# Kernel tuning notes

Measured on AMD Instinct MI355X. Metric: run time of the kernel, lower is better.

## Reference

```python
import jax, jax.numpy as jnp
import numpy as np

B, N = 128, 1369
DINO, CLIP, H = 384, 512, 8
D = CLIP // H  # head_dim = 64
EPS = 1e-5


def setup_inputs() -> dict:
    key = jax.random.key(0)
    ks = jax.random.split(key, 8)
    s_clip = 1.0 / np.sqrt(CLIP)
    s_dino = 1.0 / np.sqrt(DINO)
    return {
        "dino_features": jax.random.normal(ks[0], (B, N, DINO), jnp.float32),
        "clip_features": jax.random.normal(ks[1], (B, CLIP), jnp.float32),
        "Wq": jax.random.uniform(ks[2], (CLIP, CLIP), jnp.float32, -s_clip, s_clip),
        "bq": jnp.zeros((CLIP,), jnp.float32),
        "Wk": jax.random.uniform(ks[3], (DINO, CLIP), jnp.float32, -s_dino, s_dino),
        "bk": jnp.zeros((CLIP,), jnp.float32),
        "Wv": jax.random.uniform(ks[4], (DINO, CLIP), jnp.float32, -s_dino, s_dino),
        "bv": jnp.zeros((CLIP,), jnp.float32),
        "temperature": jnp.ones((1,), jnp.float32),
        "ln_gamma": jnp.ones((CLIP,), jnp.float32),
        "ln_beta": jnp.zeros((CLIP,), jnp.float32),
    }


def reference(dino_features, clip_features, Wq, bq, Wk, bk, Wv, bv,
              temperature, ln_gamma, ln_beta):
    # Q: (B, H, D) -- single query token from CLIP
    Q = (clip_features @ Wq + bq).reshape(B, H, D)
    # K, V: (B, N, H, D)
    K = (dino_features @ Wk + bk).reshape(B, N, H, D)
    V = (dino_features @ Wv + bv).reshape(B, N, H, D)
    scale = jnp.sqrt(jnp.float32(D)) * temperature[0]
    # attention logits over patches: (B, H, N)
    logits = jnp.einsum("bhd,bnhd->bhn", Q, K) / scale
    attn = jax.nn.softmax(logits, axis=-1)  # dropout is identity in eval mode
    out = jnp.einsum("bhn,bnhd->bhd", attn, V).reshape(B, CLIP)
    # LayerNorm over last dim
    mu = out.mean(axis=-1, keepdims=True)
    var = out.var(axis=-1, keepdims=True)
    return (out - mu) * jax.lax.rsqrt(var + EPS) * ln_gamma + ln_beta
```

## Files before the change

kernel.cpp:

```cpp
#include <hip/hip_runtime.h>
#include <math.h>
#include <stdint.h>

#define B_    128
#define N_    1369
#define DINO_ 384
#define CLIP_ 512
#define H_    8
#define CHUNKS 6
#define CH     229
#define SMP    52
#define TROWS  16

__device__ __forceinline__ float wave_sum(float v) {
  v += __shfl_xor(v, 1);  v += __shfl_xor(v, 2);  v += __shfl_xor(v, 4);
  v += __shfl_xor(v, 8);  v += __shfl_xor(v, 16); v += __shfl_xor(v, 32);
  return v;
}

__device__ __forceinline__ void gld16(const float* g, float* lds_base) {
  __builtin_amdgcn_global_load_lds(
      (const __attribute__((address_space(1))) void*)g,
      (__attribute__((address_space(3))) void*)lds_base, 16, 0, 0);
}

__global__ __launch_bounds__(256) void kq(const float* __restrict__ clip,
                                          const float* __restrict__ Wq,
                                          const float* __restrict__ bq,
                                          float* __restrict__ Q) {
  const int b = blockIdx.x;
  const int c = blockIdx.y * 256 + threadIdx.x;
  __shared__ float cl[CLIP_];
  cl[threadIdx.x] = clip[b * CLIP_ + threadIdx.x];
  cl[threadIdx.x + 256] = clip[b * CLIP_ + threadIdx.x + 256];
  __syncthreads();
  float acc = bq[c];
  #pragma unroll 8
  for (int j = 0; j < CLIP_; ++j) acc += cl[j] * Wq[j * CLIP_ + c];
  Q[b * CLIP_ + c] = acc;
}

__global__ __launch_bounds__(256) void kqk(const float* __restrict__ Wk,
                                           const float* __restrict__ Q,
                                           const float* __restrict__ temp,
                                           float* __restrict__ qkout) {
  const int b = blockIdx.x;
  const int e = blockIdx.y * 256 + threadIdx.x;
  __shared__ float qs[CLIP_];
  qs[threadIdx.x] = Q[b * CLIP_ + threadIdx.x];
  qs[threadIdx.x + 256] = Q[b * CLIP_ + threadIdx.x + 256];
  __syncthreads();
  const int h = e / DINO_;
  const int j = e - h * DINO_;
  const float rs = 1.0f / (8.0f * temp[0]);
  const float* wrow = Wk + (size_t)j * CLIP_ + h * 64;
  const float* qrow = qs + h * 64;
  float a0 = 0.f, a1 = 0.f, a2 = 0.f, a3 = 0.f;
  #pragma unroll
  for (int d = 0; d < 64; d += 4) {
    const float4 wv = *(const float4*)(wrow + d);
    const float4 qv = *(const float4*)(qrow + d);
    a0 += wv.x * qv.x;  a1 += wv.y * qv.y;
    a2 += wv.z * qv.z;  a3 += wv.w * qv.w;
  }
  qkout[(size_t)b * 3072 + e] = ((a0 + a1) + (a2 + a3)) * rs;
}

__global__ __launch_bounds__(256, 3) void kmain(const float* __restrict__ dino,
                                                const float* __restrict__ qk,
                                                float* __restrict__ ps,
                                                float* __restrict__ pl) {
  __shared__ float lds[2 * TROWS * DINO_];
  __shared__ float lm[2][H_];

  const int blk = blockIdx.x;
  const int b = blk / CHUNKS;
  const int c = blk - b * CHUNKS;
  const int n0 = c * CH;
  const int n1 = min(N_, n0 + CH);
  const int tid = threadIdx.x, w = tid >> 6, lane = tid & 63;
  const int h = lane >> 3, sl = lane & 7;
  const int off = 4 * sl;

  float qr[48];
  {
    const float* qb = qk + (size_t)b * 3072 + h * DINO_ + off;
    #pragma unroll
    for (int t = 0; t < 12; ++t) {
      const float4 v = *(const float4*)(qb + 32 * t);
      qr[4*t] = v.x; qr[4*t+1] = v.y; qr[4*t+2] = v.z; qr[4*t+3] = v.w;
    }
  }
  float s[48];
  #pragma unroll
  for (int k = 0; k < 48; ++k) s[k] = 0.0f;
  float l = 0.0f;

  const float* gdino = dino + (size_t)b * N_ * DINO_;
  const float* gclamp = dino + ((size_t)B_ * N_ * DINO_ - 4);
  const int ntiles = (n1 - n0 + TROWS - 1) / TROWS;

  {
    const float* gb = gdino + (size_t)n0 * DINO_;
    #pragma unroll
    for (int j = 0; j < 6; ++j) {
      const int seg = 6 * w + j;
      const float* g = gb + (size_t)(seg * 64 + lane) * 4;
      if (g > gclamp) g = gclamp;
      gld16(g, lds + seg * 256);
    }
  }
  __syncthreads();

  for (int t = 0; t < ntiles; ++t) {
    float* cur = lds + ((t & 1) ? TROWS * DINO_ : 0);
    float* nxt = lds + ((t & 1) ? 0 : TROWS * DINO_);
    if (t + 1 < ntiles) {
      const float* gb = gdino + (size_t)(n0 + (t + 1) * TROWS) * DINO_;
      #pragma unroll
      for (int j = 0; j < 6; ++j) {
        const int seg = 6 * w + j;
        const float* g = gb + (size_t)(seg * 64 + lane) * 4;
        if (g > gclamp) g = gclamp;
        gld16(g, nxt + seg * 256);
      }
    }
    const int tb = n0 + t * TROWS;
    #pragma unroll 1
    for (int k = 0; k < 4; ++k) {
      const int slot = w + 4 * k;
      if (tb + slot >= n1) break;
      const float* xr = cur + slot * DINO_ + off;
      float4 x[12];
      #pragma unroll
      for (int u = 0; u < 12; ++u) x[u] = *(const float4*)(xr + 32 * u);

      float a0 = 0.f, a1 = 0.f, a2 = 0.f, a3 = 0.f;
      #pragma unroll
      for (int u = 0; u < 12; ++u) {
        a0 += qr[4*u]   * x[u].x;
        a1 += qr[4*u+1] * x[u].y;
        a2 += qr[4*u+2] * x[u].z;
        a3 += qr[4*u+3] * x[u].w;
      }
      float v = (a0 + a1) + (a2 + a3);
      v += __shfl_xor(v, 1);
      v += __shfl_xor(v, 2);
      v += __shfl_xor(v, 4);
      const float p = __expf(v);
      l += p;
      #pragma unroll
      for (int u = 0; u < 12; ++u) {
        s[4*u]   += p * x[u].x;
        s[4*u+1] += p * x[u].y;
        s[4*u+2] += p * x[u].z;
        s[4*u+3] += p * x[u].w;
      }
    }
    __syncthreads();
  }

  float* sm0 = lds;
  float* sm1 = lds + 64 * SMP;
  if (w >= 2) {
    float* dst = (w == 2 ? sm0 : sm1) + lane * SMP;
    #pragma unroll
    for (int t = 0; t < 12; ++t)
      *(float4*)(dst + 4 * t) = make_float4(s[4*t], s[4*t+1], s[4*t+2], s[4*t+3]);
    if (sl == 0) lm[w - 2][h] = l;
  }
  __syncthreads();
  if (w < 2) {
    const float* src = (w == 0 ? sm0 : sm1) + lane * SMP;
    #pragma unroll
    for (int t = 0; t < 12; ++t) {
      const float4 v = *(const float4*)(src + 4 * t);
      s[4*t] += v.x; s[4*t+1] += v.y; s[4*t+2] += v.z; s[4*t+3] += v.w;
    }
    l += lm[w][h];
  }
  __syncthreads();
  if (w == 1) {
    float* dst = sm0 + lane * SMP;
    #pragma unroll
    for (int t = 0; t < 12; ++t)
      *(float4*)(dst + 4 * t) = make_float4(s[4*t], s[4*t+1], s[4*t+2], s[4*t+3]);
    if (sl == 0) lm[0][h] = l;
  }
  __syncthreads();
  if (w == 0) {
    const float* src = sm0 + lane * SMP;
    #pragma unroll
    for (int t = 0; t < 12; ++t) {
      const float4 v = *(const float4*)(src + 4 * t);
      s[4*t] += v.x; s[4*t+1] += v.y; s[4*t+2] += v.z; s[4*t+3] += v.w;
    }
    l += lm[0][h];
    float* pso = ps + (size_t)blk * 3072 + h * DINO_ + off;
    #pragma unroll
    for (int t = 0; t < 12; ++t)
      *(float4*)(pso + 32 * t) = make_float4(s[4*t], s[4*t+1], s[4*t+2], s[4*t+3]);
    if (sl == 0) pl[blk * H_ + h] = l;
  }
}

__global__ __launch_bounds__(512) void kmf(const float* __restrict__ ps,
                                           const float* __restrict__ pl,
                                           const float* __restrict__ Wv,
                                           const float* __restrict__ bv,
                                           const float* __restrict__ gamma,
                                           const float* __restrict__ beta,
                                           float* __restrict__ out) {
  const int b = blockIdx.x, tid = threadIdx.x;
  __shared__ float sfl[3072];
  __shared__ float rL[H_];
  float a[6];
  #pragma unroll
  for (int r = 0; r < 6; ++r) {
    const int e = tid + 512 * r;
    float acc = 0.0f;
    #pragma unroll
    for (int cc = 0; cc < CHUNKS; ++cc)
      acc += ps[(size_t)(b * CHUNKS + cc) * 3072 + e];
    a[r] = acc;
  }
  if (tid < H_) {
    float L = 0.0f;
    #pragma unroll
    for (int cc = 0; cc < CHUNKS; ++cc) L += pl[(b * CHUNKS + cc) * H_ + tid];
    rL[tid] = 1.0f / L;
  }
  __syncthreads();
  #pragma unroll
  for (int r = 0; r < 6; ++r) {
    const int e = tid + 512 * r;
    sfl[e] = a[r] * rL[e / DINO_];
  }
  __syncthreads();
  const int w = tid >> 6, lane = tid & 63;
  const float* srow = sfl + (tid >> 6) * DINO_;
  float acc = bv[tid];
  #pragma unroll 8
  for (int d = 0; d < DINO_; ++d) acc += srow[d] * Wv[d * CLIP_ + tid];
  float sum = wave_sum(acc);
  float sq  = wave_sum(acc * acc);
  __shared__ float rS[8], rQ[8];
  if (lane == 0) { rS[w] = sum; rQ[w] = sq; }
  __syncthreads();
  float tot = 0.0f, totq = 0.0f;
  #pragma unroll
  for (int i = 0; i < 8; ++i) { tot += rS[i]; totq += rQ[i]; }
  const float mu = tot * (1.0f / 512.0f);
  const float var = totq * (1.0f / 512.0f) - mu * mu;
  const float rstd = rsqrtf(var + 1e-5f);
  out[(size_t)b * CLIP_ + tid] = (acc - mu) * rstd * gamma[tid] + beta[tid];
}

extern "C" void kernel_launch(void* const* d_in, const int* in_sizes, int n_in,
                              void* d_out, int out_size, void* d_ws, size_t ws_size,
                              hipStream_t stream) {
  const float* dino  = (const float*)d_in[0];
  const float* clip  = (const float*)d_in[1];
  const float* Wq    = (const float*)d_in[2];
  const float* bq    = (const float*)d_in[3];
  const float* Wk    = (const float*)d_in[4];
  const float* Wv    = (const float*)d_in[6];
  const float* bv    = (const float*)d_in[7];
  const float* temp  = (const float*)d_in[8];
  const float* gamma = (const float*)d_in[9];
  const float* beta  = (const float*)d_in[10];
  float* out = (float*)d_out;

  float* ws  = (float*)d_ws;
  float* Q   = ws;
  float* qkb = Q   + 65536;
  float* ps  = qkb + 393216;
  float* pl  = ps  + 2359296;

  kq   <<<dim3(B_, 2),  256, 0, stream>>>(clip, Wq, bq, Q);
  kqk  <<<dim3(B_, 12), 256, 0, stream>>>(Wk, Q, temp, qkb);
  kmain<<<B_ * CHUNKS,  256, 0, stream>>>(dino, qkb, ps, pl);
  kmf  <<<B_,           512, 0, stream>>>(ps, pl, Wv, bv, gamma, beta, out);
}
```

Measured before the change: 474.3 us.

## Fuse Q projection kernels and remap main-loop lanes to reduce shuffles and LDS traffic

Merges the Q projection and Q·Wk fold into one kernel per batch, removing a launch and the Q round trip through global memory. The main attention kernel uses 8 chunks of 172 rows with 12-row tiles and 4 blocks per CU. Each lane now holds 12 input features for 4 heads instead of 48 features for one head, so each row reads only 3 float4 from LDS. Logits are reduced with a butterfly of selective shuffles across heads. This cuts LDS read bandwidth and adds parallelism, at the cost of more shuffle instructions, a serialized fused pre-kernel, and more partial sums for the final kernel to combine.

New measurement: 511.4 us. +7.8%, slower.

```diff
diff --git a/kernel.cpp b/kernel.cpp
--- a/kernel.cpp
+++ b/kernel.cpp
@@ -7,10 +7,11 @@
 #define DINO_ 384
 #define CLIP_ 512
 #define H_    8
-#define CHUNKS 6
-#define CH     229
+#define CHUNKS 8
+#define CH     172
+#define TROWS  12
+#define SEGS   18
 #define SMP    52
-#define TROWS  16
 
 __device__ __forceinline__ float wave_sum(float v) {
   v += __shfl_xor(v, 1);  v += __shfl_xor(v, 2);  v += __shfl_xor(v, 4);
@@ -24,49 +25,47 @@
       (__attribute__((address_space(3))) void*)lds_base, 16, 0, 0);
 }
 
-__global__ __launch_bounds__(256) void kq(const float* __restrict__ clip,
-                                          const float* __restrict__ Wq,
-                                          const float* __restrict__ bq,
-                                          float* __restrict__ Q) {
-  const int b = blockIdx.x;
-  const int c = blockIdx.y * 256 + threadIdx.x;
-  __shared__ float cl[CLIP_];
-  cl[threadIdx.x] = clip[b * CLIP_ + threadIdx.x];
-  cl[threadIdx.x + 256] = clip[b * CLIP_ + threadIdx.x + 256];
-  __syncthreads();
-  float acc = bq[c];
-  #pragma unroll 8
-  for (int j = 0; j < CLIP_; ++j) acc += cl[j] * Wq[j * CLIP_ + c];
-  Q[b * CLIP_ + c] = acc;
-}
-
-__global__ __launch_bounds__(256) void kqk(const float* __restrict__ Wk,
-                                           const float* __restrict__ Q,
+__global__ __launch_bounds__(256) void kqq(const float* __restrict__ clip,
+                                           const float* __restrict__ Wq,
+                                           const float* __restrict__ bq,
+                                           const float* __restrict__ Wk,
                                            const float* __restrict__ temp,
                                            float* __restrict__ qkout) {
-  const int b = blockIdx.x;
-  const int e = blockIdx.y * 256 + threadIdx.x;
-  __shared__ float qs[CLIP_];
-  qs[threadIdx.x] = Q[b * CLIP_ + threadIdx.x];
-  qs[threadIdx.x + 256] = Q[b * CLIP_ + threadIdx.x + 256];
-  __syncthreads();
-  const int h = e / DINO_;
-  const int j = e - h * DINO_;
+  const int b = blockIdx.x, tid = threadIdx.x;
+  __shared__ float cl[CLIP_], qs[CLIP_];
+  cl[tid] = clip[b * CLIP_ + tid];
+  cl[tid + 256] = clip[b * CLIP_ + tid + 256];
+  __syncthreads();
+  #pragma unroll
+  for (int half = 0; half < 2; ++half) {
+    const int cc = tid + 256 * half;
+    float acc = bq[cc];
+    #pragma unroll 8
+    for (int j = 0; j < CLIP_; ++j) acc += cl[j] * Wq[j * CLIP_ + cc];
+    qs[cc] = acc;
+  }
+  __syncthreads();
   const float rs = 1.0f / (8.0f * temp[0]);
-  const float* wrow = Wk + (size_t)j * CLIP_ + h * 64;
-  const float* qrow = qs + h * 64;
-  float a0 = 0.f, a1 = 0.f, a2 = 0.f, a3 = 0.f;
-  #pragma unroll
-  for (int d = 0; d < 64; d += 4) {
-    const float4 wv = *(const float4*)(wrow + d);
-    const float4 qv = *(const float4*)(qrow + d);
-    a0 += wv.x * qv.x;  a1 += wv.y * qv.y;
-    a2 += wv.z * qv.z;  a3 += wv.w * qv.w;
-  }
-  qkout[(size_t)b * 3072 + e] = ((a0 + a1) + (a2 + a3)) * rs;
-}
-
-__global__ __launch_bounds__(256, 3) void kmain(const float* __restrict__ dino,
+  #pragma unroll 1
+  for (int r = 0; r < 12; ++r) {
+    const int e = tid + 256 * r;
+    const int h = e / DINO_;
+    const int j = e - h * DINO_;
+    const float* wrow = Wk + (size_t)j * CLIP_ + h * 64;
+    const float* qrow = qs + h * 64;
+    float a0 = 0.f, a1 = 0.f, a2 = 0.f, a3 = 0.f;
+    #pragma unroll
+    for (int d = 0; d < 64; d += 4) {
+      const float4 wv = *(const float4*)(wrow + d);
+      const float4 qv = *(const float4*)(qrow + d);
+      a0 += wv.x * qv.x;  a1 += wv.y * qv.y;
+      a2 += wv.z * qv.z;  a3 += wv.w * qv.w;
+    }
+    qkout[(size_t)b * 3072 + e] = ((a0 + a1) + (a2 + a3)) * rs;
+  }
+}
+
+__global__ __launch_bounds__(256, 4) void kmain(const float* __restrict__ dino,
                                                 const float* __restrict__ qk,
                                                 float* __restrict__ ps,
                                                 float* __restrict__ pl) {
@@ -74,26 +73,32 @@
   __shared__ float lm[2][H_];
 
   const int blk = blockIdx.x;
-  const int b = blk / CHUNKS;
-  const int c = blk - b * CHUNKS;
+  const int b = blk >> 3;
+  const int c = blk & 7;
   const int n0 = c * CH;
   const int n1 = min(N_, n0 + CH);
   const int tid = threadIdx.x, w = tid >> 6, lane = tid & 63;
-  const int h = lane >> 3, sl = lane & 7;
-  const int off = 4 * sl;
-
-  float qr[48];
+  const int m = lane & 31;
+  const int G = lane >> 5;
+  const int b4 = (lane >> 4) & 1, b3 = (lane >> 3) & 1;
+  const int hO = 2 * b4 + b3;
+
+  float qr[4][12];
   {
-    const float* qb = qk + (size_t)b * 3072 + h * DINO_ + off;
-    #pragma unroll
-    for (int t = 0; t < 12; ++t) {
-      const float4 v = *(const float4*)(qb + 32 * t);
-      qr[4*t] = v.x; qr[4*t+1] = v.y; qr[4*t+2] = v.z; qr[4*t+3] = v.w;
-    }
-  }
-  float s[48];
-  #pragma unroll
-  for (int k = 0; k < 48; ++k) s[k] = 0.0f;
+    const float* qb = qk + (size_t)b * 3072 + (G * 4) * DINO_ + 4 * m;
+    #pragma unroll
+    for (int j = 0; j < 4; ++j)
+      #pragma unroll
+      for (int t = 0; t < 3; ++t) {
+        const float4 v = *(const float4*)(qb + j * DINO_ + 128 * t);
+        qr[j][4*t] = v.x; qr[j][4*t+1] = v.y; qr[j][4*t+2] = v.z; qr[j][4*t+3] = v.w;
+      }
+  }
+  float s[4][12];
+  #pragma unroll
+  for (int j = 0; j < 4; ++j)
+    #pragma unroll
+    for (int q = 0; q < 12; ++q) s[j][q] = 0.0f;
   float l = 0.0f;
 
   const float* gdino = dino + (size_t)b * N_ * DINO_;
@@ -102,12 +107,10 @@
 
   {
     const float* gb = gdino + (size_t)n0 * DINO_;
-    #pragma unroll
-    for (int j = 0; j < 6; ++j) {
-      const int seg = 6 * w + j;
-      const float* g = gb + (size_t)(seg * 64 + lane) * 4;
+    for (int sg = w; sg < SEGS; sg += 4) {
+      const float* g = gb + sg * 256 + 4 * lane;
       if (g > gclamp) g = gclamp;
-      gld16(g, lds + seg * 256);
+      gld16(g, lds + sg * 256);
     }
   }
   __syncthreads();
@@ -117,45 +120,61 @@
     float* nxt = lds + ((t & 1) ? 0 : TROWS * DINO_);
     if (t + 1 < ntiles) {
       const float* gb = gdino + (size_t)(n0 + (t + 1) * TROWS) * DINO_;
-      #pragma unroll
-      for (int j = 0; j < 6; ++j) {
-        const int seg = 6 * w + j;
-        const float* g = gb + (size_t)(seg * 64 + lane) * 4;
+      for (int sg = w; sg < SEGS; sg += 4) {
+        const float* g = gb + sg * 256 + 4 * lane;
         if (g > gclamp) g = gclamp;
-        gld16(g, nxt + seg * 256);
+        gld16(g, nxt + sg * 256);
       }
     }
     const int tb = n0 + t * TROWS;
     #pragma unroll 1
-    for (int k = 0; k < 4; ++k) {
+    for (int k = 0; k < 3; ++k) {
       const int slot = w + 4 * k;
       if (tb + slot >= n1) break;
-      const float* xr = cur + slot * DINO_ + off;
-      float4 x[12];
-      #pragma unroll
-      for (int u = 0; u < 12; ++u) x[u] = *(const float4*)(xr + 32 * u);
-
-      float a0 = 0.f, a1 = 0.f, a2 = 0.f, a3 = 0.f;
-      #pragma unroll
-      for (int u = 0; u < 12; ++u) {
-        a0 += qr[4*u]   * x[u].x;
-        a1 += qr[4*u+1] * x[u].y;
-        a2 += qr[4*u+2] * x[u].z;
-        a3 += qr[4*u+3] * x[u].w;
-      }
-      float v = (a0 + a1) + (a2 + a3);
-      v += __shfl_xor(v, 1);
-      v += __shfl_xor(v, 2);
-      v += __shfl_xor(v, 4);
-      const float p = __expf(v);
+      const float* xr = cur + slot * DINO_ + 4 * m;
+      const float4 x0 = *(const float4*)(xr);
+      const float4 x1 = *(const float4*)(xr + 128);
+      const float4 x2 = *(const float4*)(xr + 256);
+      const float xv[12] = {x0.x, x0.y, x0.z, x0.w,
+                            x1.x, x1.y, x1.z, x1.w,
+                            x2.x, x2.y, x2.z, x2.w};
+      float va[4];
+      #pragma unroll
+      for (int j = 0; j < 4; ++j) {
+        float a = 0.f, bacc = 0.f;
+        #pragma unroll
+        for (int q = 0; q < 12; q += 2) {
+          a    += qr[j][q]     * xv[q];
+          bacc += qr[j][q + 1] * xv[q + 1];
+        }
+        va[j] = a + bacc;
+      }
+      float c0, c1;
+      {
+        const float t0 = __shfl_xor(va[0], 16), t1 = __shfl_xor(va[1], 16);
+        const float t2 = __shfl_xor(va[2], 16), t3 = __shfl_xor(va[3], 16);
+        c0 = b4 ? va[2] + t2 : va[0] + t0;
+        c1 = b4 ? va[3] + t3 : va[1] + t1;
+      }
+      float d;
+      {
+        const float u0 = __shfl_xor(c0, 8), u1 = __shfl_xor(c1, 8);
+        d = b3 ? c1 + u1 : c0 + u0;
+      }
+      d += __shfl_xor(d, 4);
+      d += __shfl_xor(d, 2);
+      d += __shfl_xor(d, 1);
+      const float p = __expf(d);
       l += p;
-      #pragma unroll
-      for (int u = 0; u < 12; ++u) {
-        s[4*u]   += p * x[u].x;
-        s[4*u+1] += p * x[u].y;
-        s[4*u+2] += p * x[u].z;
-        s[4*u+3] += p * x[u].w;
-      }
+      float P[4];
+      P[0] = p;
+      P[1] = __shfl_xor(p, 8);
+      P[2] = __shfl_xor(p, 16);
+      P[3] = __shfl_xor(P[1], 16);
+      #pragma unroll
+      for (int j = 0; j < 4; ++j)
+        #pragma unroll
+        for (int q = 0; q < 12; ++q) s[j][q] += P[j] * xv[q];
     }
     __syncthreads();
   }
@@ -165,42 +184,58 @@
   if (w >= 2) {
     float* dst = (w == 2 ? sm0 : sm1) + lane * SMP;
     #pragma unroll
-    for (int t = 0; t < 12; ++t)
-      *(float4*)(dst + 4 * t) = make_float4(s[4*t], s[4*t+1], s[4*t+2], s[4*t+3]);
-    if (sl == 0) lm[w - 2][h] = l;
+    for (int j = 0; j < 4; ++j)
+      #pragma unroll
+      for (int t = 0; t < 3; ++t)
+        *(float4*)(dst + j * 12 + 4 * t) =
+            make_float4(s[j][4*t], s[j][4*t+1], s[j][4*t+2], s[j][4*t+3]);
+    if ((lane & 7) == 0) lm[w - 2][4 * G + hO] = l;
   }
   __syncthreads();
   if (w < 2) {
     const float* src = (w == 0 ? sm0 : sm1) + lane * SMP;
     #pragma unroll
-    for (int t = 0; t < 12; ++t) {
-      const float4 v = *(const float4*)(src + 4 * t);
-      s[4*t] += v.x; s[4*t+1] += v.y; s[4*t+2] += v.z; s[4*t+3] += v.w;
-    }
-    l += lm[w][h];
+    for (int j = 0; j < 4; ++j)
+      #pragma unroll
+      for (int t = 0; t < 3; ++t) {
+        const float4 v = *(const float4*)(src + j * 12 + 4 * t);
+        s[j][4*t] += v.x; s[j][4*t+1] += v.y; s[j][4*t+2] += v.z; s[j][4*t+3] += v.w;
+      }
+    l += lm[w][4 * G + hO];
   }
   __syncthreads();
   if (w == 1) {
     float* dst = sm0 + lane * SMP;
     #pragma unroll
-    for (int t = 0; t < 12; ++t)
-      *(float4*)(dst + 4 * t) = make_float4(s[4*t], s[4*t+1], s[4*t+2], s[4*t+3]);
-    if (sl == 0) lm[0][h] = l;
+    for (int j = 0; j < 4; ++j)
+      #pragma unroll
+      for (int t = 0; t < 3; ++t)
+        *(float4*)(dst + j * 12 + 4 * t) =
+            make_float4(s[j][4*t], s[j][4*t+1], s[j][4*t+2], s[j][4*t+3]);
+    if ((lane & 7) == 0) lm[0][4 * G + hO] = l;
   }
   __syncthreads();
   if (w == 0) {
     const float* src = sm0 + lane * SMP;
     #pragma unroll
-    for (int t = 0; t < 12; ++t) {
-      const float4 v = *(const float4*)(src + 4 * t);
-      s[4*t] += v.x; s[4*t+1] += v.y; s[4*t+2] += v.z; s[4*t+3] += v.w;
-    }
-    l += lm[0][h];
-    float* pso = ps + (size_t)blk * 3072 + h * DINO_ + off;
-    #pragma unroll
-    for (int t = 0; t < 12; ++t)
-      *(float4*)(pso + 32 * t) = make_float4(s[4*t], s[4*t+1], s[4*t+2], s[4*t+3]);
-    if (sl == 0) pl[blk * H_ + h] = l;
+    for (int j = 0; j < 4; ++j)
+      #pragma unroll
+      for (int t = 0; t < 3; ++t) {
+        const float4 v = *(const float4*)(src + j * 12 + 4 * t);
+        s[j][4*t] += v.x; s[j][4*t+1] += v.y; s[j][4*t+2] += v.z; s[j][4*t+3] += v.w;
+      }
+    l += lm[0][4 * G + hO];
+    float* pso = ps + (size_t)blk * 3072;
+    #pragma unroll
+    for (int j = 0; j < 4; ++j) {
+      const int h = 4 * G + (hO ^ j);
+      float* o = pso + h * DINO_ + 4 * m;
+      #pragma unroll
+      for (int t = 0; t < 3; ++t)
+        *(float4*)(o + 128 * t) =
+            make_float4(s[j][4*t], s[j][4*t+1], s[j][4*t+2], s[j][4*t+3]);
+    }
+    if ((lane & 7) == 0) pl[blk * H_ + 4 * G + hO] = l;
   }
 }
 
@@ -272,13 +307,11 @@
   float* out = (float*)d_out;
 
   float* ws  = (float*)d_ws;
-  float* Q   = ws;
-  float* qkb = Q   + 65536;
+  float* qkb = ws;
   float* ps  = qkb + 393216;
-  float* pl  = ps  + 2359296;
-
-  kq   <<<dim3(B_, 2),  256, 0, stream>>>(clip, Wq, bq, Q);
-  kqk  <<<dim3(B_, 12), 256, 0, stream>>>(Wk, Q, temp, qkb);
+  float* pl  = ps  + 3145728;
+
+  kqq  <<<B_,           256, 0, stream>>>(clip, Wq, bq, Wk, temp, qkb);
   kmain<<<B_ * CHUNKS,  256, 0, stream>>>(dino, qkb, ps, pl);
   kmf  <<<B_,           512, 0, stream>>>(ps, pl, Wv, bv, gamma, beta, out);
 }
```
